# Performance work log

Hardware: AMD Instinct MI355X
Metric: run time of the kernel (lower is better)

Reference implementation:

```python
import jax, jax.numpy as jnp
import numpy as np
from functools import partial

EPS = 1e-3  # keras LayerNormalization default epsilon

def _conv_same(inp, w):
    # inp: [B,H,W,Cin], w: [k,k,Cin,Cout]
    return jax.lax.conv_general_dilated(
        inp, w, window_strides=(1, 1), padding='SAME',
        dimension_numbers=('NHWC', 'HWIO', 'NHWC'))

def _hard_sigmoid(x):
    # keras recurrent_activation default for ConvLSTM2D
    return jnp.clip(0.2 * x + 0.5, 0.0, 1.0)

def setup_inputs() -> dict:
    key = jax.random.key(0)
    k1, k2, k3 = jax.random.split(key, 3)
    B, T, H, W, C, F, K = 4, 16, 64, 64, 32, 64, 3
    x = jax.random.normal(k1, (B, T, H, W, C), dtype=jnp.float32)
    gamma = jnp.ones((C,), jnp.float32)
    beta = jnp.zeros((C,), jnp.float32)
    # gate order i, f, c, o stacked along output channels (keras convention)
    Wx = jax.random.normal(k2, (K, K, C, 4 * F), dtype=jnp.float32) * 0.05
    Wh = jax.random.normal(k3, (K, K, F, 4 * F), dtype=jnp.float32) * 0.05
    b = jnp.zeros((4 * F,), jnp.float32)
    return {"x": x, "gamma": gamma, "beta": beta, "Wx": Wx, "Wh": Wh, "b": b}

def reference(x, gamma, beta, Wx, Wh, b):
    B, T, H, W, C = x.shape
    F = Wh.shape[2]
    # LayerNorm over channel axis
    mu = jnp.mean(x, axis=-1, keepdims=True)
    var = jnp.var(x, axis=-1, keepdims=True)
    xn = (x - mu) * jax.lax.rsqrt(var + EPS) * gamma + beta

    # Precompute input-to-gate convs for all timesteps at once (time folded into batch)
    zx = _conv_same(xn.reshape(B * T, H, W, C), Wx) + b  # [B*T,H,W,4F]
    zx = zx.reshape(B, T, H, W, 4 * F).transpose(1, 0, 2, 3, 4)  # [T,B,H,W,4F]

    def step(carry, zxt):
        h, c = carry
        z = zxt + _conv_same(h, Wh)
        zi, zf, zc, zo = jnp.split(z, 4, axis=-1)
        i = _hard_sigmoid(zi)
        f = _hard_sigmoid(zf)
        c = f * c + i * jnp.tanh(zc)
        o = _hard_sigmoid(zo)
        h = o * jnp.tanh(c)
        return (h, c), h

    h0 = jnp.zeros((B, H, W, F), x.dtype)
    c0 = jnp.zeros((B, H, W, F), x.dtype)
    _, hs = jax.lax.scan(step, (h0, c0), zx)  # hs: [T,B,H,W,F]
    y = hs.transpose(1, 0, 2, 3, 4)  # [B,T,H,W,F] (return_sequences=True)

    # MaxPool3D pool_size=(1,2,2), stride = pool_size, VALID padding
    y = jax.lax.reduce_window(
        y, -jnp.inf, jax.lax.max,
        window_dimensions=(1, 1, 2, 2, 1),
        window_strides=(1, 1, 2, 2, 1),
        padding='VALID')
    return y
```

## Files before the change

### kernel.cpp

```cpp
#include <hip/hip_runtime.h>
#include <hip/hip_fp16.h>

typedef _Float16 f16;
typedef _Float16 f16x8 __attribute__((ext_vector_type(8)));
typedef float f32x4 __attribute__((ext_vector_type(4)));
typedef unsigned long long ull;

#define BB 4
#define TT 16
#define HH 64
#define WW 64
#define CC 32
#define FF 64
#define GG 256

__device__ __forceinline__ float hsig(float z) {
    return fminf(fmaxf(0.2f * z + 0.5f, 0.f), 1.f);
}
__device__ __forceinline__ float tanh_fast(float x) {
    return 1.f - 2.f / (__expf(2.f * x) + 1.f);
}

__device__ __forceinline__ void async_copy16(const void* g, void* l) {
    __builtin_amdgcn_global_load_lds(
        (const __attribute__((address_space(1))) unsigned*)g,
        (__attribute__((address_space(3))) unsigned*)l, 16, 0, 0);
}

__global__ void wprep_kernel(const float* __restrict__ wx, const float* __restrict__ wh,
                             f16* __restrict__ wcat) {
    int e = blockIdx.x * 256 + threadIdx.x;
    if (e < 9 * CC * GG) {
        int n = e & 255, k = e >> 8;
        int p = k / 96, r = k % 96;
        wcat[((p * 12 + (r >> 3)) * 256 + n) * 8 + (r & 7)] = (f16)wx[e];
    } else {
        e -= 9 * CC * GG;
        if (e < 9 * FF * GG) {
            int n = e & 255, k = 288 + (e >> 8);
            int p = k / 96, r = k % 96;
            wcat[((p * 12 + (r >> 3)) * 256 + n) * 8 + (r & 7)] = (f16)wh[e];
        }
    }
}

__global__ __launch_bounds__(512, 2)
void fused_kernel(const float* __restrict__ x, const float* __restrict__ gamma,
                  const float* __restrict__ beta, const f16* __restrict__ wcat,
                  const float* __restrict__ bs, f16* __restrict__ halo,
                  float* __restrict__ out, unsigned* __restrict__ flags) {
    __shared__ __align__(16) f16 patches[3 * 7200];
    __shared__ __align__(16) f16 wbuf[2 * 24576];
    __shared__ float sg[CC], sb[CC];

    f16* xpatch = patches;
    int tid = threadIdx.x;
    int tile = blockIdx.x;
    int bb = tile >> 6, ty = (tile >> 3) & 7, tx = tile & 7;
    int lane = tid & 63, w = tid >> 6;
    int wm = w >> 2, nhalf = (w >> 1) & 1, wn = w & 1;
    int quad = lane >> 4, noff = lane & 15;

    if (tid < CC) sg[tid] = gamma[tid];
    else if (tid < 2 * CC) sb[tid - CC] = beta[tid - CC];

    for (int i = tid; i < 2700; i += 512)
        ((f16x8*)patches)[i] = (f16x8){0, 0, 0, 0, 0, 0, 0, 0};

    const char* gw[6];
#pragma unroll
    for (int i = 0; i < 6; i++) {
        int g = w * 6 + i;
        gw[i] = (const char*)wcat + ((size_t)(g >> 2) * 256 + (g & 3) * 64 + lane) * 16;
    }

    int fch = (nhalf << 5) + (wn << 4) + noff;
    float b_i = bs[fch], b_f = bs[64 + fch], b_c = bs[128 + fch], b_o = bs[192 + fch];

    float creg[2][4];
#pragma unroll
    for (int mt = 0; mt < 2; mt++)
#pragma unroll
        for (int r = 0; r < 4; r++) creg[mt][r] = 0.f;

    int mrow[2];
#pragma unroll
    for (int mt = 0; mt < 2; mt++) {
        int m = (wm << 5) + (mt << 4) + noff;
        mrow[mt] = ((m >> 3) * 10 + (m & 7)) * 72 + (quad << 3);
    }
    int rB[4];
#pragma unroll
    for (int cls = 0; cls < 4; cls++) rB[cls] = ((cls << 6) + fch) << 3;

    __syncthreads();

#pragma unroll
    for (int i = 0; i < 6; i++) {
        int g = w * 6 + i;
        async_copy16(gw[i], &wbuf[(g >> 2) * 2048 + (g & 3) * 512]);
    }

    for (int t = 0; t < TT; t++) {
        f16* hp_cur = patches + 7200 + (t & 1) * 7200;
        f16* hp_nxt = patches + 7200 + ((t + 1) & 1) * 7200;
        f16* wrd0 = &wbuf[(t & 1) * 24576];
        f16* wrd1 = &wbuf[((t + 1) & 1) * 24576];

        if (tid < 200) {
            int pix = tid >> 1, part = tid & 1;
            int py = pix / 10, px_ = pix % 10;
            int gy = ty * 8 - 1 + py, gx = tx * 8 - 1 + px_;
            if (gy >= 0 && gy < HH && gx >= 0 && gx < WW) {
                const float* xp = x + ((size_t)(bb * TT + t) * (HH * WW)
                                       + gy * WW + gx) * CC + part * 16;
                float v[16];
                float s = 0.f, s2 = 0.f;
#pragma unroll
                for (int j = 0; j < 4; j++) {
                    float4 t4 = *(const float4*)(xp + j * 4);
                    v[j * 4] = t4.x; v[j * 4 + 1] = t4.y; v[j * 4 + 2] = t4.z; v[j * 4 + 3] = t4.w;
                    s += t4.x + t4.y + t4.z + t4.w;
                    s2 += t4.x * t4.x + t4.y * t4.y + t4.z * t4.z + t4.w * t4.w;
                }
                s += __shfl_xor(s, 1);
                s2 += __shfl_xor(s2, 1);
                float mu = s * (1.f / CC);
                float var = s2 * (1.f / CC) - mu * mu;
                float rs = rsqrtf(var + 1e-3f);
                f16 o16[16];
#pragma unroll
                for (int c = 0; c < 16; c++)
                    o16[c] = (f16)((v[c] - mu) * rs * sg[part * 16 + c] + sb[part * 16 + c]);
                f16x8* d = (f16x8*)&xpatch[pix * 72 + part * 16];
                d[0] = *(f16x8*)&o16[0];
                d[1] = *(f16x8*)&o16[8];
            }
        }

        f32x4 acc[2][4];
#pragma unroll
        for (int i = 0; i < 2; i++)
#pragma unroll
            for (int j = 0; j < 4; j++) acc[i][j] = (f32x4){0.f, 0.f, 0.f, 0.f};

#pragma unroll
        for (int p = 0; p < 9; ++p) {
            __syncthreads();
            {
                int nc = (p == 8) ? 0 : p + 1;
                f16* wdst = (p & 1) ? wrd0 : wrd1;
#pragma unroll
                for (int i = 0; i < 6; i++) {
                    int g = w * 6 + i;
                    async_copy16(gw[i] + (size_t)nc * 49152,
                                 &wdst[(g >> 2) * 2048 + (g & 3) * 512]);
                }
            }
            const f16* wbp = (p & 1) ? wrd1 : wrd0;
#pragma unroll
            for (int cw = 0; cw < 3; ++cw) {
                int c = p * 3 + cw;
                bool isx = c < 9;
                int hc = c - 9;
                int tap = isx ? c : (hc >> 1);
                int coff = isx ? 0 : ((hc & 1) << 5);
                const f16* ap = isx ? xpatch : hp_cur;
                int dy = tap / 3, dx = tap % 3;
                int toff = (dy * 10 + dx) * 72 + coff;
                f16x8 a[2];
#pragma unroll
                for (int mt = 0; mt < 2; mt++)
                    a[mt] = *(const f16x8*)&ap[mrow[mt] + toff];
#pragma unroll
                for (int cls = 0; cls < 4; cls++) {
                    f16x8 bf = *(const f16x8*)&wbp[((cw << 2) + quad) * 2048 + rB[cls]];
                    acc[0][cls] = __builtin_amdgcn_mfma_f32_16x16x32_f16(a[0], bf, acc[0][cls], 0, 0, 0);
                    acc[1][cls] = __builtin_amdgcn_mfma_f32_16x16x32_f16(a[1], bf, acc[1][cls], 0, 0, 0);
                }
            }
            if (p == 2 && t > 0 && tid >= 256 && tid < 400) {
                int e = tid - 256;
                int hx = e >> 2, quarter = e & 3;
                int py, px_;
                if (hx < 10)      { py = 0; px_ = hx; }
                else if (hx < 20) { py = 9; px_ = hx - 10; }
                else if (hx < 28) { py = 1 + (hx - 20); px_ = 0; }
                else              { py = 1 + (hx - 28); px_ = 9; }
                int gy = ty * 8 - 1 + py, gx = tx * 8 - 1 + px_;
                if (gy >= 0 && gy < HH && gx >= 0 && gx < WW) {
                    int nb = bb * 64 + ((gy >> 3) << 3) + (gx >> 3);
                    while (__hip_atomic_load(&flags[nb], __ATOMIC_RELAXED,
                                             __HIP_MEMORY_SCOPE_AGENT) < (unsigned)t)
                        __builtin_amdgcn_s_sleep(1);
                    const ull* src = (const ull*)(halo + ((size_t)(t * BB + bb) * (HH * WW)
                                                         + gy * WW + gx) * FF) + quarter * 4;
                    f16* dst = &hp_cur[(py * 10 + px_) * 72 + quarter * 16];
#pragma unroll
                    for (int j = 0; j < 4; j++) {
                        ull vv = __hip_atomic_load(src + j, __ATOMIC_RELAXED,
                                                   __HIP_MEMORY_SCOPE_AGENT);
                        *(ull*)(dst + j * 4) = vv;
                    }
                }
            }
        }

#pragma unroll
        for (int mt = 0; mt < 2; mt++) {
#pragma unroll
            for (int r = 0; r < 4; r++) {
                int m = (wm << 5) + (mt << 4) + (quad << 2) + r;
                int py8 = m >> 3, px8 = m & 7;
                float zi = acc[mt][0][r] + b_i;
                float zf = acc[mt][1][r] + b_f;
                float zc = acc[mt][2][r] + b_c;
                float zo = acc[mt][3][r] + b_o;
                float ig = hsig(zi), fg = hsig(zf), og = hsig(zo);
                float cn = fg * creg[mt][r] + ig * tanh_fast(zc);
                creg[mt][r] = cn;
                f16 hval = (f16)(og * tanh_fast(cn));
                hp_nxt[((py8 + 1) * 10 + px8 + 1) * 72 + fch] = hval;
                if (py8 == 0 || py8 == 7 || px8 == 0 || px8 == 7) {
                    union { f16 f; unsigned short u; } cvt; cvt.f = hval;
                    unsigned short* hp = (unsigned short*)halo
                        + ((size_t)((t + 1) * BB + bb) * (HH * WW)
                           + (ty * 8 + py8) * WW + (tx * 8 + px8)) * FF + fch;
                    __hip_atomic_store(hp, cvt.u, __ATOMIC_RELAXED, __HIP_MEMORY_SCOPE_AGENT);
                }
            }
        }
        __syncthreads();
        if (tid == 0)
            __hip_atomic_store(&flags[tile], (unsigned)(t + 1), __ATOMIC_RELAXED,
                               __HIP_MEMORY_SCOPE_AGENT);

        {
            int o = tid * 2;
            int f0 = o & 63;
            int ox2 = (o >> 6) & 3, oy2 = (o >> 8) & 3;
            int row = 1 + oy2 * 2, col = 1 + ox2 * 2;
            const f16* hb = &hp_nxt[(row * 10 + col) * 72 + f0];
            float v0 = fmaxf(fmaxf((float)hb[0], (float)hb[72]),
                             fmaxf((float)hb[720], (float)hb[792]));
            float v1 = fmaxf(fmaxf((float)hb[1], (float)hb[73]),
                             fmaxf((float)hb[721], (float)hb[793]));
            size_t ofs = (((size_t)(bb * TT + t) * 32 + (ty * 4 + oy2)) * 32
                          + (tx * 4 + ox2)) * 64 + f0;
            float2 v2; v2.x = v0; v2.y = v1;
            *(float2*)(out + ofs) = v2;
        }
    }
}

__global__ void ln_kernel(const float* __restrict__ x,
                          const float* __restrict__ gamma,
                          const float* __restrict__ beta,
                          f16* __restrict__ xn) {
    __shared__ float sg[CC], sb[CC];
    if (threadIdx.x < CC) sg[threadIdx.x] = gamma[threadIdx.x];
    else if (threadIdx.x < 2 * CC) sb[threadIdx.x - CC] = beta[threadIdx.x - CC];
    __syncthreads();
    int q = blockIdx.x * 256 + threadIdx.x;
    const float* xp = x + (size_t)q * CC;
    float v[CC];
    float s = 0.f, s2 = 0.f;
#pragma unroll
    for (int c = 0; c < CC; c += 4) {
        float4 t4 = *(const float4*)(xp + c);
        v[c] = t4.x; v[c + 1] = t4.y; v[c + 2] = t4.z; v[c + 3] = t4.w;
        s += t4.x + t4.y + t4.z + t4.w;
        s2 += t4.x * t4.x + t4.y * t4.y + t4.z * t4.z + t4.w * t4.w;
    }
    float mu = s * (1.f / CC);
    float var = s2 * (1.f / CC) - mu * mu;
    float rs = rsqrtf(var + 1e-3f);
    f16 o[CC];
#pragma unroll
    for (int c = 0; c < CC; c++)
        o[c] = (f16)((v[c] - mu) * rs * sg[c] + sb[c]);
    f16x8* d = (f16x8*)(xn + (size_t)q * CC);
#pragma unroll
    for (int c = 0; c < 4; c++) d[c] = *(f16x8*)&o[c * 8];
}

__global__ __launch_bounds__(256, 2)
void step_kernel(const f16* __restrict__ xn, const f16* __restrict__ wcat,
                 const float* __restrict__ bs,
                 float* __restrict__ cst, f16* __restrict__ hs, int t) {
    __shared__ __align__(16) f16 xpatch[100 * 72];
    __shared__ __align__(16) f16 hpatch[100 * 72];
    __shared__ __align__(16) f16 wbuf[2 * 12288];

    int tile = blockIdx.x >> 1, nhalf = blockIdx.x & 1;
    int bb = tile >> 6, ty = (tile >> 3) & 7, tx = tile & 7;
    int tid = threadIdx.x;
    int lane = tid & 63, w = tid >> 6;
    int wm = w >> 1, wn = w & 1;
    int quad = lane >> 4, noff = lane & 15;

    const char* gw[6];
#pragma unroll
    for (int i = 0; i < 6; i++) {
        int g = w * 6 + i;
        int hb = g & 1;
        int gate = (((hb << 1) + (lane >> 5)) << 6) + (nhalf << 5) + (lane & 31);
        gw[i] = (const char*)wcat + ((size_t)(g >> 1) * 256 + gate) * 16;
    }
#pragma unroll
    for (int i = 0; i < 6; i++) {
        int g = w * 6 + i;
        async_copy16(gw[i], &wbuf[(g >> 1) * 1024 + (g & 1) * 512]);
    }

    const f16* xslice = xn + (size_t)(bb * TT + t) * (HH * WW) * CC;
    const f16* hprev = hs + (size_t)t * (BB * HH * WW * FF);
    f16* hnew = hs + (size_t)(t + 1) * (BB * HH * WW * FF);

    if (tid < 200) {
        int pix = tid >> 1, part = tid & 1;
        int py = pix / 10, px = pix % 10;
        int y = ty * 8 - 1 + py, x = tx * 8 - 1 + px;
        bool in = (y >= 0 && y < HH && x >= 0 && x < WW);
        f16x8 z = {0, 0, 0, 0, 0, 0, 0, 0};
        {
            f16x8* d = (f16x8*)&xpatch[pix * 72 + part * 16];
            if (in) {
                const f16x8* s = (const f16x8*)(xslice + ((size_t)y * WW + x) * CC + part * 16);
                d[0] = s[0]; d[1] = s[1];
            } else { d[0] = z; d[1] = z; }
        }
        {
            f16x8* d = (f16x8*)&hpatch[pix * 72 + part * 32];
            if (in) {
                const f16x8* s = (const f16x8*)(hprev + ((size_t)(bb * HH + y) * WW + x) * FF + part * 32);
                d[0] = s[0]; d[1] = s[1]; d[2] = s[2]; d[3] = s[3];
            } else { d[0] = z; d[1] = z; d[2] = z; d[3] = z; }
        }
    }

    int fch = (nhalf << 5) + (wn << 4) + noff;
    float b_i = bs[fch], b_f = bs[64 + fch], b_c = bs[128 + fch], b_o = bs[192 + fch];

    f32x4 acc[2][4];
#pragma unroll
    for (int i = 0; i < 2; i++)
#pragma unroll
        for (int j = 0; j < 4; j++) acc[i][j] = (f32x4){0.f, 0.f, 0.f, 0.f};

#pragma unroll
    for (int p = 0; p < 9; ++p) {
        __syncthreads();
        if (p < 8) {
#pragma unroll
            for (int i = 0; i < 6; i++) {
                int g = w * 6 + i;
                async_copy16(gw[i] + (size_t)(p + 1) * 49152,
                             &wbuf[((p + 1) & 1) * 12288 + (g >> 1) * 1024 + (g & 1) * 512]);
            }
        }
        const f16* wb = &wbuf[(p & 1) * 12288];
#pragma unroll
        for (int cw = 0; cw < 3; ++cw) {
            int c = p * 3 + cw;
            bool isx = c < 9;
            int hc = c - 9;
            int tap = isx ? c : (hc >> 1);
            int coff = isx ? 0 : ((hc & 1) << 5);
            const f16* ap = isx ? xpatch : hpatch;
            int dy = tap / 3, dx = tap % 3;
            f16x8 a[2];
#pragma unroll
            for (int mt = 0; mt < 2; mt++) {
                int m = (wm << 5) + (mt << 4) + noff;
                int pp = ((m >> 3) + dy) * 10 + (m & 7) + dx;
                a[mt] = *(const f16x8*)&ap[pp * 72 + coff + (quad << 3)];
            }
#pragma unroll
            for (int cls = 0; cls < 4; cls++) {
                f16x8 bf = *(const f16x8*)&wb[((cw << 2) + quad) * 1024 + (((cls << 5) + (wn << 4) + noff) << 3)];
                acc[0][cls] = __builtin_amdgcn_mfma_f32_16x16x32_f16(a[0], bf, acc[0][cls], 0, 0, 0);
                acc[1][cls] = __builtin_amdgcn_mfma_f32_16x16x32_f16(a[1], bf, acc[1][cls], 0, 0, 0);
            }
        }
    }

#pragma unroll
    for (int mt = 0; mt < 2; mt++) {
#pragma unroll
        for (int r = 0; r < 4; r++) {
            int m = (wm << 5) + (mt << 4) + (quad << 2) + r;
            int y = ty * 8 + (m >> 3), x = tx * 8 + (m & 7);
            size_t p = (size_t)(bb * HH + y) * WW + x;
            float zi = acc[mt][0][r] + b_i;
            float zf = acc[mt][1][r] + b_f;
            float zc = acc[mt][2][r] + b_c;
            float zo = acc[mt][3][r] + b_o;
            float ig = hsig(zi), fg = hsig(zf), og = hsig(zo);
            float cold = cst[p * FF + fch];
            float cn = fg * cold + ig * tanh_fast(zc);
            cst[p * FF + fch] = cn;
            hnew[p * FF + fch] = (f16)(og * tanh_fast(cn));
        }
    }
}

__global__ void pool_kernel(const f16* __restrict__ hs, float* __restrict__ out) {
    int idx = blockIdx.x * 256 + threadIdx.x;
    int f = idx & 63;
    int ox = (idx >> 6) & 31;
    int oy = (idx >> 11) & 31;
    int t = (idx >> 16) & 15;
    int bb = idx >> 20;
    const f16* base = hs + (size_t)(t + 1) * (BB * HH * WW * FF)
                    + ((size_t)(bb * HH + oy * 2) * WW + ox * 2) * FF + f;
    float v0 = (float)base[0];
    float v1 = (float)base[FF];
    float v2 = (float)base[WW * FF];
    float v3 = (float)base[WW * FF + FF];
    out[idx] = fmaxf(fmaxf(v0, v1), fmaxf(v2, v3));
}

extern "C" void kernel_launch(void* const* d_in, const int* in_sizes, int n_in,
                              void* d_out, int out_size, void* d_ws, size_t ws_size,
                              hipStream_t stream) {
    const float* x = (const float*)d_in[0];
    const float* gamma = (const float*)d_in[1];
    const float* beta = (const float*)d_in[2];
    const float* wx = (const float*)d_in[3];
    const float* wh = (const float*)d_in[4];
    const float* bs = (const float*)d_in[5];
    float* out = (float*)d_out;

    char* ws = (char*)d_ws;
    f16* xn = (f16*)ws;
    f16* wcat = (f16*)(ws + 16777216);
    float* cst = (float*)(ws + 17219584);
    f16* hs = (f16*)(ws + 21413888);
    unsigned* flags = (unsigned*)cst;

    hipMemsetAsync(flags, 0, 256 * 4, stream);
    wprep_kernel<<<864, 256, 0, stream>>>(wx, wh, wcat);

    void* args[8];
    args[0] = (void*)&x;
    args[1] = (void*)&gamma;
    args[2] = (void*)&beta;
    args[3] = (void*)&wcat;
    args[4] = (void*)&bs;
    args[5] = (void*)&hs;
    args[6] = (void*)&out;
    args[7] = (void*)&flags;
    hipError_t err = hipLaunchCooperativeKernel((const void*)fused_kernel, dim3(256),
                                                dim3(512), args, 0, stream);
    if (err != hipSuccess) {
        (void)hipGetLastError();
        hipMemsetAsync(cst, 0, (size_t)BB * HH * WW * FF * 4, stream);
        hipMemsetAsync(hs, 0, (size_t)BB * HH * WW * FF * 2, stream);
        ln_kernel<<<1024, 256, 0, stream>>>(x, gamma, beta, xn);
        for (int t = 0; t < TT; t++)
            step_kernel<<<512, 256, 0, stream>>>(xn, wcat, bs, cst, hs, t);
        pool_kernel<<<16384, 256, 0, stream>>>(hs, out);
    }
}
```

Measured before the change: 295.3 us.

## Split work by gate-channel quarter on 16x16 spatial tiles in fused ConvLSTM

Blocks now own a 16x16 spatial tile and one quarter of the F channels (all four gates for 16 channels), in place of an 8x8 tile covering every channel. The weight layout is split per quarter with an XOR swizzle to avoid LDS bank conflicts. Each block writes its full h to global and reloads the whole 18x18 patch every step, and the max-pool and the next step's LayerNorm staging move into the tap loop. This cuts per-block weight traffic and halo overhead, at the cost of more global h traffic, finer-grained flag waits, and a 4x redundant LayerNorm across the quarter blocks.

```diff
diff --git a/kernel.cpp b/kernel.cpp
--- a/kernel.cpp
+++ b/kernel.cpp
@@ -28,53 +28,86 @@
 }
 
 __global__ void wprep_kernel(const float* __restrict__ wx, const float* __restrict__ wh,
-                             f16* __restrict__ wcat) {
-    int e = blockIdx.x * 256 + threadIdx.x;
-    if (e < 9 * CC * GG) {
-        int n = e & 255, k = e >> 8;
-        int p = k / 96, r = k % 96;
-        wcat[((p * 12 + (r >> 3)) * 256 + n) * 8 + (r & 7)] = (f16)wx[e];
+                             f16* __restrict__ wcatA, f16* __restrict__ wcatB) {
+    int e0 = blockIdx.x * 256 + threadIdx.x;
+    float val; int k, ng;
+    if (e0 < 9 * CC * GG) {
+        ng = e0 & 255; k = e0 >> 8; val = wx[e0];
     } else {
-        e -= 9 * CC * GG;
-        if (e < 9 * FF * GG) {
-            int n = e & 255, k = 288 + (e >> 8);
-            int p = k / 96, r = k % 96;
-            wcat[((p * 12 + (r >> 3)) * 256 + n) * 8 + (r & 7)] = (f16)wh[e];
+        int e = e0 - 9 * CC * GG;
+        ng = e & 255; k = 288 + (e >> 8); val = wh[e];
+    }
+    int p = k / 96, r = k % 96, j = r >> 3, el = r & 7;
+    wcatB[((p * 12 + j) * 256 + ng) * 8 + el] = (f16)val;
+    int q = (ng >> 4) & 3;
+    int n = ((ng >> 6) << 4) | (ng & 15);
+    int slot = n ^ ((j & 3) << 1);
+    wcatA[(((q * 9 + p) * 12 + j) * 64 + slot) * 8 + el] = (f16)val;
+}
+
+__device__ __forceinline__ void stage_x_ln(const float* __restrict__ x, int bb, int t,
+                                           int tY, int tX, int tid,
+                                           const float* sg, const float* sb,
+                                           f16* xpatch) {
+    if (tid < 324) {
+        int py = tid / 18, pxx = tid - py * 18;
+        int gy = tY * 16 - 1 + py, gx = tX * 16 - 1 + pxx;
+        if (gy >= 0 && gy < HH && gx >= 0 && gx < WW) {
+            const float* xp = x + ((size_t)(bb * TT + t) * (HH * WW) + gy * WW + gx) * CC;
+            float v[CC];
+            float s = 0.f, s2 = 0.f;
+#pragma unroll
+            for (int c = 0; c < CC; c += 4) {
+                float4 t4 = *(const float4*)(xp + c);
+                v[c] = t4.x; v[c + 1] = t4.y; v[c + 2] = t4.z; v[c + 3] = t4.w;
+                s += t4.x + t4.y + t4.z + t4.w;
+                s2 += t4.x * t4.x + t4.y * t4.y + t4.z * t4.z + t4.w * t4.w;
+            }
+            float mu = s * (1.f / CC);
+            float var = s2 * (1.f / CC) - mu * mu;
+            float rs = rsqrtf(var + 1e-3f);
+            f16 o[CC];
+#pragma unroll
+            for (int c = 0; c < CC; c++)
+                o[c] = (f16)((v[c] - mu) * rs * sg[c] + sb[c]);
+            *(f16x8*)&xpatch[tid * 40]      = *(f16x8*)&o[0];
+            *(f16x8*)&xpatch[tid * 40 + 8]  = *(f16x8*)&o[8];
+            *(f16x8*)&xpatch[tid * 40 + 16] = *(f16x8*)&o[16];
+            *(f16x8*)&xpatch[tid * 40 + 24] = *(f16x8*)&o[24];
         }
     }
 }
 
 __global__ __launch_bounds__(512, 2)
 void fused_kernel(const float* __restrict__ x, const float* __restrict__ gamma,
-                  const float* __restrict__ beta, const f16* __restrict__ wcat,
+                  const float* __restrict__ beta, const f16* __restrict__ wcatA,
                   const float* __restrict__ bs, f16* __restrict__ halo,
                   float* __restrict__ out, unsigned* __restrict__ flags) {
-    __shared__ __align__(16) f16 patches[3 * 7200];
-    __shared__ __align__(16) f16 wbuf[2 * 24576];
+    __shared__ __align__(16) f16 xpatch[324 * 40];
+    __shared__ __align__(16) f16 hpatch[324 * 72];
+    __shared__ __align__(16) f16 wbuf[2 * 6144];
     __shared__ float sg[CC], sb[CC];
 
-    f16* xpatch = patches;
     int tid = threadIdx.x;
-    int tile = blockIdx.x;
-    int bb = tile >> 6, ty = (tile >> 3) & 7, tx = tile & 7;
+    int bid = blockIdx.x;
+    int Q = bid & 3, tl = bid >> 2;
+    int bb = tl >> 4, tY = (tl >> 2) & 3, tX = tl & 3;
     int lane = tid & 63, w = tid >> 6;
-    int wm = w >> 2, nhalf = (w >> 1) & 1, wn = w & 1;
     int quad = lane >> 4, noff = lane & 15;
 
     if (tid < CC) sg[tid] = gamma[tid];
     else if (tid < 2 * CC) sb[tid - CC] = beta[tid - CC];
 
-    for (int i = tid; i < 2700; i += 512)
-        ((f16x8*)patches)[i] = (f16x8){0, 0, 0, 0, 0, 0, 0, 0};
-
-    const char* gw[6];
-#pragma unroll
-    for (int i = 0; i < 6; i++) {
-        int g = w * 6 + i;
-        gw[i] = (const char*)wcat + ((size_t)(g >> 2) * 256 + (g & 3) * 64 + lane) * 16;
-    }
-
-    int fch = (nhalf << 5) + (wn << 4) + noff;
+    {
+        f16x8 z8 = {0, 0, 0, 0, 0, 0, 0, 0};
+        for (int i = tid; i < 1620; i += 512) ((f16x8*)xpatch)[i] = z8;
+        for (int i = tid; i < 2916; i += 512) ((f16x8*)hpatch)[i] = z8;
+    }
+
+    const char* gw0 = (const char*)wcatA + (size_t)Q * 110592 + w * 1024 + lane * 16;
+    const char* gw1 = gw0 + 8192;
+
+    int fch = (Q << 4) + noff;
     float b_i = bs[fch], b_f = bs[64 + fch], b_c = bs[128 + fch], b_o = bs[192 + fch];
 
     float creg[2][4];
@@ -83,60 +116,23 @@
 #pragma unroll
         for (int r = 0; r < 4; r++) creg[mt][r] = 0.f;
 
-    int mrow[2];
+    int arow[2], hrow[2];
 #pragma unroll
     for (int mt = 0; mt < 2; mt++) {
-        int m = (wm << 5) + (mt << 4) + noff;
-        mrow[mt] = ((m >> 3) * 10 + (m & 7)) * 72 + (quad << 3);
-    }
-    int rB[4];
-#pragma unroll
-    for (int cls = 0; cls < 4; cls++) rB[cls] = ((cls << 6) + fch) << 3;
+        arow[mt] = ((w * 2 + mt) * 18 + noff) * 40 + (quad << 3);
+        hrow[mt] = ((w * 2 + mt) * 18 + noff) * 72 + (quad << 3);
+    }
+    int qB = quad * 512 + ((noff ^ (quad << 1)) << 3);
 
     __syncthreads();
 
-#pragma unroll
-    for (int i = 0; i < 6; i++) {
-        int g = w * 6 + i;
-        async_copy16(gw[i], &wbuf[(g >> 2) * 2048 + (g & 3) * 512]);
-    }
+    async_copy16(gw0, &wbuf[w * 512]);
+    if (w < 4) async_copy16(gw1, &wbuf[4096 + w * 512]);
+    stage_x_ln(x, bb, 0, tY, tX, tid, sg, sb, xpatch);
 
     for (int t = 0; t < TT; t++) {
-        f16* hp_cur = patches + 7200 + (t & 1) * 7200;
-        f16* hp_nxt = patches + 7200 + ((t + 1) & 1) * 7200;
-        f16* wrd0 = &wbuf[(t & 1) * 24576];
-        f16* wrd1 = &wbuf[((t + 1) & 1) * 24576];
-
-        if (tid < 200) {
-            int pix = tid >> 1, part = tid & 1;
-            int py = pix / 10, px_ = pix % 10;
-            int gy = ty * 8 - 1 + py, gx = tx * 8 - 1 + px_;
-            if (gy >= 0 && gy < HH && gx >= 0 && gx < WW) {
-                const float* xp = x + ((size_t)(bb * TT + t) * (HH * WW)
-                                       + gy * WW + gx) * CC + part * 16;
-                float v[16];
-                float s = 0.f, s2 = 0.f;
-#pragma unroll
-                for (int j = 0; j < 4; j++) {
-                    float4 t4 = *(const float4*)(xp + j * 4);
-                    v[j * 4] = t4.x; v[j * 4 + 1] = t4.y; v[j * 4 + 2] = t4.z; v[j * 4 + 3] = t4.w;
-                    s += t4.x + t4.y + t4.z + t4.w;
-                    s2 += t4.x * t4.x + t4.y * t4.y + t4.z * t4.z + t4.w * t4.w;
-                }
-                s += __shfl_xor(s, 1);
-                s2 += __shfl_xor(s2, 1);
-                float mu = s * (1.f / CC);
-                float var = s2 * (1.f / CC) - mu * mu;
-                float rs = rsqrtf(var + 1e-3f);
-                f16 o16[16];
-#pragma unroll
-                for (int c = 0; c < 16; c++)
-                    o16[c] = (f16)((v[c] - mu) * rs * sg[part * 16 + c] + sb[part * 16 + c]);
-                f16x8* d = (f16x8*)&xpatch[pix * 72 + part * 16];
-                d[0] = *(f16x8*)&o16[0];
-                d[1] = *(f16x8*)&o16[8];
-            }
-        }
+        f16* wrd0 = &wbuf[(t & 1) * 6144];
+        f16* wrd1 = &wbuf[((t + 1) & 1) * 6144];
 
         f32x4 acc[2][4];
 #pragma unroll
@@ -150,12 +146,8 @@
             {
                 int nc = (p == 8) ? 0 : p + 1;
                 f16* wdst = (p & 1) ? wrd0 : wrd1;
-#pragma unroll
-                for (int i = 0; i < 6; i++) {
-                    int g = w * 6 + i;
-                    async_copy16(gw[i] + (size_t)nc * 49152,
-                                 &wdst[(g >> 2) * 2048 + (g & 3) * 512]);
-                }
+                async_copy16(gw0 + nc * 12288, &wdst[w * 512]);
+                if (w < 4) async_copy16(gw1 + nc * 12288, &wdst[4096 + w * 512]);
             }
             const f16* wbp = (p & 1) ? wrd1 : wrd0;
 #pragma unroll
@@ -165,53 +157,76 @@
                 int hc = c - 9;
                 int tap = isx ? c : (hc >> 1);
                 int coff = isx ? 0 : ((hc & 1) << 5);
-                const f16* ap = isx ? xpatch : hp_cur;
                 int dy = tap / 3, dx = tap % 3;
-                int toff = (dy * 10 + dx) * 72 + coff;
                 f16x8 a[2];
 #pragma unroll
                 for (int mt = 0; mt < 2; mt++)
-                    a[mt] = *(const f16x8*)&ap[mrow[mt] + toff];
+                    a[mt] = isx
+                        ? *(const f16x8*)&xpatch[arow[mt] + (dy * 18 + dx) * 40]
+                        : *(const f16x8*)&hpatch[hrow[mt] + (dy * 18 + dx) * 72 + coff];
 #pragma unroll
                 for (int cls = 0; cls < 4; cls++) {
-                    f16x8 bf = *(const f16x8*)&wbp[((cw << 2) + quad) * 2048 + rB[cls]];
+                    f16x8 bf = *(const f16x8*)&wbp[qB + cw * 2048 + cls * 128];
                     acc[0][cls] = __builtin_amdgcn_mfma_f32_16x16x32_f16(a[0], bf, acc[0][cls], 0, 0, 0);
                     acc[1][cls] = __builtin_amdgcn_mfma_f32_16x16x32_f16(a[1], bf, acc[1][cls], 0, 0, 0);
                 }
             }
-            if (p == 2 && t > 0 && tid >= 256 && tid < 400) {
-                int e = tid - 256;
-                int hx = e >> 2, quarter = e & 3;
-                int py, px_;
-                if (hx < 10)      { py = 0; px_ = hx; }
-                else if (hx < 20) { py = 9; px_ = hx - 10; }
-                else if (hx < 28) { py = 1 + (hx - 20); px_ = 0; }
-                else              { py = 1 + (hx - 28); px_ = 9; }
-                int gy = ty * 8 - 1 + py, gx = tx * 8 - 1 + px_;
-                if (gy >= 0 && gy < HH && gx >= 0 && gx < WW) {
-                    int nb = bb * 64 + ((gy >> 3) << 3) + (gx >> 3);
-                    while (__hip_atomic_load(&flags[nb], __ATOMIC_RELAXED,
-                                             __HIP_MEMORY_SCOPE_AGENT) < (unsigned)t)
-                        __builtin_amdgcn_s_sleep(1);
-                    const ull* src = (const ull*)(halo + ((size_t)(t * BB + bb) * (HH * WW)
-                                                         + gy * WW + gx) * FF) + quarter * 4;
-                    f16* dst = &hp_cur[(py * 10 + px_) * 72 + quarter * 16];
-#pragma unroll
-                    for (int j = 0; j < 4; j++) {
-                        ull vv = __hip_atomic_load(src + j, __ATOMIC_RELAXED,
-                                                   __HIP_MEMORY_SCOPE_AGENT);
-                        *(ull*)(dst + j * 4) = vv;
+            if (p == 2 && t > 0) {
+#pragma unroll
+                for (int k2 = 0; k2 < 3; k2++) {
+                    int tau = tid + k2 * 512;
+                    if (tau < 1296) {
+                        int pxi = tau >> 2, grp = tau & 3;
+                        int py = pxi / 18, pxx = pxi - py * 18;
+                        int gy = tY * 16 - 1 + py, gx = tX * 16 - 1 + pxx;
+                        if (gy >= 0 && gy < HH && gx >= 0 && gx < WW) {
+                            int nb = ((bb * 16 + (gy >> 4) * 4 + (gx >> 4)) << 2) | grp;
+                            while (__hip_atomic_load(&flags[nb], __ATOMIC_RELAXED,
+                                                     __HIP_MEMORY_SCOPE_AGENT) < (unsigned)t)
+                                __builtin_amdgcn_s_sleep(1);
+                            const ull* src = (const ull*)(halo
+                                + ((size_t)(t * BB + bb) * (HH * WW) + gy * WW + gx) * FF
+                                + grp * 16);
+                            ull v0 = __hip_atomic_load(src, __ATOMIC_RELAXED,
+                                                       __HIP_MEMORY_SCOPE_AGENT);
+                            ull v1 = __hip_atomic_load(src + 1, __ATOMIC_RELAXED,
+                                                       __HIP_MEMORY_SCOPE_AGENT);
+                            ull v2 = __hip_atomic_load(src + 2, __ATOMIC_RELAXED,
+                                                       __HIP_MEMORY_SCOPE_AGENT);
+                            ull v3 = __hip_atomic_load(src + 3, __ATOMIC_RELAXED,
+                                                       __HIP_MEMORY_SCOPE_AGENT);
+                            ull* dst = (ull*)&hpatch[pxi * 72 + grp * 16];
+                            dst[0] = v0; dst[1] = v1; dst[2] = v2; dst[3] = v3;
+                        }
                     }
                 }
             }
+            if (p == 3 && t > 0) {
+                int a_ = tid >> 6, b_ = (tid >> 3) & 7, ch = (tid & 7) << 3;
+                const f16* h00 = &hpatch[((1 + 2 * a_) * 18 + 1 + 2 * b_) * 72 + ch];
+                f16x8 q00 = *(const f16x8*)h00;
+                f16x8 q01 = *(const f16x8*)(h00 + 72);
+                f16x8 q10 = *(const f16x8*)(h00 + 18 * 72);
+                f16x8 q11 = *(const f16x8*)(h00 + 18 * 72 + 72);
+                float o8[8];
+#pragma unroll
+                for (int j = 0; j < 8; j++)
+                    o8[j] = fmaxf(fmaxf((float)q00[j], (float)q01[j]),
+                                  fmaxf((float)q10[j], (float)q11[j]));
+                size_t ofs = ((((size_t)bb * TT + (t - 1)) * 32 + tY * 8 + a_) * 32
+                              + (tX * 8 + b_)) * 64 + ch;
+                *(float4*)(out + ofs) = *(float4*)&o8[0];
+                *(float4*)(out + ofs + 4) = *(float4*)&o8[4];
+            }
+            if (p == 4 && t + 1 < TT)
+                stage_x_ln(x, bb, t + 1, tY, tX, tid, sg, sb, xpatch);
         }
 
 #pragma unroll
         for (int mt = 0; mt < 2; mt++) {
 #pragma unroll
             for (int r = 0; r < 4; r++) {
-                int m = (wm << 5) + (mt << 4) + (quad << 2) + r;
-                int py8 = m >> 3, px8 = m & 7;
+                int gy = tY * 16 + w * 2 + mt, gx = tX * 16 + (quad << 2) + r;
                 float zi = acc[mt][0][r] + b_i;
                 float zf = acc[mt][1][r] + b_f;
                 float zc = acc[mt][2][r] + b_c;
@@ -219,37 +234,47 @@
                 float ig = hsig(zi), fg = hsig(zf), og = hsig(zo);
                 float cn = fg * creg[mt][r] + ig * tanh_fast(zc);
                 creg[mt][r] = cn;
-                f16 hval = (f16)(og * tanh_fast(cn));
-                hp_nxt[((py8 + 1) * 10 + px8 + 1) * 72 + fch] = hval;
-                if (py8 == 0 || py8 == 7 || px8 == 0 || px8 == 7) {
-                    union { f16 f; unsigned short u; } cvt; cvt.f = hval;
-                    unsigned short* hp = (unsigned short*)halo
-                        + ((size_t)((t + 1) * BB + bb) * (HH * WW)
-                           + (ty * 8 + py8) * WW + (tx * 8 + px8)) * FF + fch;
-                    __hip_atomic_store(hp, cvt.u, __ATOMIC_RELAXED, __HIP_MEMORY_SCOPE_AGENT);
-                }
+                union { f16 f; unsigned short u; } cvt;
+                cvt.f = (f16)(og * tanh_fast(cn));
+                unsigned short* hp = (unsigned short*)halo
+                    + ((size_t)((t + 1) * BB + bb) * (HH * WW) + gy * WW + gx) * FF + fch;
+                __hip_atomic_store(hp, cvt.u, __ATOMIC_RELAXED, __HIP_MEMORY_SCOPE_AGENT);
             }
         }
         __syncthreads();
         if (tid == 0)
-            __hip_atomic_store(&flags[tile], (unsigned)(t + 1), __ATOMIC_RELAXED,
+            __hip_atomic_store(&flags[bid], (unsigned)(t + 1), __ATOMIC_RELAXED,
                                __HIP_MEMORY_SCOPE_AGENT);
-
-        {
-            int o = tid * 2;
-            int f0 = o & 63;
-            int ox2 = (o >> 6) & 3, oy2 = (o >> 8) & 3;
-            int row = 1 + oy2 * 2, col = 1 + ox2 * 2;
-            const f16* hb = &hp_nxt[(row * 10 + col) * 72 + f0];
-            float v0 = fmaxf(fmaxf((float)hb[0], (float)hb[72]),
-                             fmaxf((float)hb[720], (float)hb[792]));
-            float v1 = fmaxf(fmaxf((float)hb[1], (float)hb[73]),
-                             fmaxf((float)hb[721], (float)hb[793]));
-            size_t ofs = (((size_t)(bb * TT + t) * 32 + (ty * 4 + oy2)) * 32
-                          + (tx * 4 + ox2)) * 64 + f0;
-            float2 v2; v2.x = v0; v2.y = v1;
-            *(float2*)(out + ofs) = v2;
-        }
+    }
+
+    if (tid < 4) {
+        while (__hip_atomic_load(&flags[(tl << 2) | tid], __ATOMIC_RELAXED,
+                                 __HIP_MEMORY_SCOPE_AGENT) < (unsigned)TT)
+            __builtin_amdgcn_s_sleep(2);
+    }
+    __syncthreads();
+    {
+        int a_ = tid >> 6, b_ = (tid >> 3) & 7, ch = (tid & 7) << 3;
+        float o8[8];
+#pragma unroll
+        for (int j = 0; j < 8; j++) o8[j] = -1e30f;
+#pragma unroll
+        for (int dy2 = 0; dy2 < 2; dy2++)
+#pragma unroll
+            for (int dx2 = 0; dx2 < 2; dx2++) {
+                int gy = tY * 16 + 2 * a_ + dy2, gx = tX * 16 + 2 * b_ + dx2;
+                const ull* src = (const ull*)(halo
+                    + ((size_t)(TT * BB + bb) * (HH * WW) + gy * WW + gx) * FF + ch);
+                ull v0 = __hip_atomic_load(src, __ATOMIC_RELAXED, __HIP_MEMORY_SCOPE_AGENT);
+                ull v1 = __hip_atomic_load(src + 1, __ATOMIC_RELAXED, __HIP_MEMORY_SCOPE_AGENT);
+                f16 tmp[8];
+                *(ull*)&tmp[0] = v0; *(ull*)&tmp[4] = v1;
+#pragma unroll
+                for (int j = 0; j < 8; j++) o8[j] = fmaxf(o8[j], (float)tmp[j]);
+            }
+        size_t ofs = ((((size_t)bb * TT + 15) * 32 + tY * 8 + a_) * 32 + (tX * 8 + b_)) * 64 + ch;
+        *(float4*)(out + ofs) = *(float4*)&o8[0];
+        *(float4*)(out + ofs + 4) = *(float4*)&o8[4];
     }
 }
 
@@ -434,19 +459,20 @@
 
     char* ws = (char*)d_ws;
     f16* xn = (f16*)ws;
-    f16* wcat = (f16*)(ws + 16777216);
+    f16* wcatB = (f16*)(ws + 16777216);
     float* cst = (float*)(ws + 17219584);
     f16* hs = (f16*)(ws + 21413888);
+    f16* wcatA = (f16*)(ws + 57065472);
     unsigned* flags = (unsigned*)cst;
 
     hipMemsetAsync(flags, 0, 256 * 4, stream);
-    wprep_kernel<<<864, 256, 0, stream>>>(wx, wh, wcat);
+    wprep_kernel<<<864, 256, 0, stream>>>(wx, wh, wcatA, wcatB);
 
     void* args[8];
     args[0] = (void*)&x;
     args[1] = (void*)&gamma;
     args[2] = (void*)&beta;
-    args[3] = (void*)&wcat;
+    args[3] = (void*)&wcatA;
     args[4] = (void*)&bs;
     args[5] = (void*)&hs;
     args[6] = (void*)&out;
@@ -459,7 +485,7 @@
         hipMemsetAsync(hs, 0, (size_t)BB * HH * WW * FF * 2, stream);
         ln_kernel<<<1024, 256, 0, stream>>>(x, gamma, beta, xn);
         for (int t = 0; t < TT; t++)
-            step_kernel<<<512, 256, 0, stream>>>(xn, wcat, bs, cst, hs, t);
+            step_kernel<<<512, 256, 0, stream>>>(xn, wcatB, bs, cst, hs, t);
         pool_kernel<<<16384, 256, 0, stream>>>(hs, out);
     }
 }
```

Result: slower. 332.2 us (+12.5%).

## Swizzle weight layout in LDS and prefetch next-step LayerNorm x-patch mid-step

Applied to the files above, without the earlier changes.

Adds a second, XOR-swizzled weight copy (wcatF) whose slot index is permuted by the K-chunk, so that B-fragment reads from LDS by different quads hit different banks. The fused kernel reads B through the matching swizzled offsets, while the fallback path keeps the original layout. LayerNorm staging of the next timestep's x patch moves from the start of each step to the middle of the tap loop (after p==4, once the x taps are consumed), to overlap global loads with MFMA work. This needs another workspace region and relies on the x patch no longer being read after p==2.

```diff
diff --git a/kernel.cpp b/kernel.cpp
--- a/kernel.cpp
+++ b/kernel.cpp
@@ -28,25 +28,60 @@
 }
 
 __global__ void wprep_kernel(const float* __restrict__ wx, const float* __restrict__ wh,
-                             f16* __restrict__ wcat) {
-    int e = blockIdx.x * 256 + threadIdx.x;
-    if (e < 9 * CC * GG) {
-        int n = e & 255, k = e >> 8;
-        int p = k / 96, r = k % 96;
-        wcat[((p * 12 + (r >> 3)) * 256 + n) * 8 + (r & 7)] = (f16)wx[e];
+                             f16* __restrict__ wcatF, f16* __restrict__ wcatB) {
+    int e0 = blockIdx.x * 256 + threadIdx.x;
+    float val; int k, ng;
+    if (e0 < 9 * CC * GG) {
+        ng = e0 & 255; k = e0 >> 8; val = wx[e0];
     } else {
-        e -= 9 * CC * GG;
-        if (e < 9 * FF * GG) {
-            int n = e & 255, k = 288 + (e >> 8);
-            int p = k / 96, r = k % 96;
-            wcat[((p * 12 + (r >> 3)) * 256 + n) * 8 + (r & 7)] = (f16)wh[e];
+        int e = e0 - 9 * CC * GG;
+        ng = e & 255; k = 288 + (e >> 8); val = wh[e];
+    }
+    int p = k / 96, r = k % 96, j = r >> 3, el = r & 7;
+    wcatB[((p * 12 + j) * 256 + ng) * 8 + el] = (f16)val;
+    int slot = ng ^ ((j & 3) << 1);
+    wcatF[((p * 12 + j) * 256 + slot) * 8 + el] = (f16)val;
+}
+
+__device__ __forceinline__ void stage_x_ln(const float* __restrict__ x, int bb, int t,
+                                           int ty, int tx, int tid,
+                                           const float* sg, const float* sb,
+                                           f16* __restrict__ xpatch) {
+    if (tid < 200) {
+        int pix = tid >> 1, part = tid & 1;
+        int py = pix / 10, px_ = pix % 10;
+        int gy = ty * 8 - 1 + py, gx = tx * 8 - 1 + px_;
+        if (gy >= 0 && gy < HH && gx >= 0 && gx < WW) {
+            const float* xp = x + ((size_t)(bb * TT + t) * (HH * WW)
+                                   + gy * WW + gx) * CC + part * 16;
+            float v[16];
+            float s = 0.f, s2 = 0.f;
+#pragma unroll
+            for (int j = 0; j < 4; j++) {
+                float4 t4 = *(const float4*)(xp + j * 4);
+                v[j * 4] = t4.x; v[j * 4 + 1] = t4.y; v[j * 4 + 2] = t4.z; v[j * 4 + 3] = t4.w;
+                s += t4.x + t4.y + t4.z + t4.w;
+                s2 += t4.x * t4.x + t4.y * t4.y + t4.z * t4.z + t4.w * t4.w;
+            }
+            s += __shfl_xor(s, 1);
+            s2 += __shfl_xor(s2, 1);
+            float mu = s * (1.f / CC);
+            float var = s2 * (1.f / CC) - mu * mu;
+            float rs = rsqrtf(var + 1e-3f);
+            f16 o16[16];
+#pragma unroll
+            for (int c = 0; c < 16; c++)
+                o16[c] = (f16)((v[c] - mu) * rs * sg[part * 16 + c] + sb[part * 16 + c]);
+            f16x8* d = (f16x8*)&xpatch[pix * 72 + part * 16];
+            d[0] = *(f16x8*)&o16[0];
+            d[1] = *(f16x8*)&o16[8];
         }
     }
 }
 
 __global__ __launch_bounds__(512, 2)
 void fused_kernel(const float* __restrict__ x, const float* __restrict__ gamma,
-                  const float* __restrict__ beta, const f16* __restrict__ wcat,
+                  const float* __restrict__ beta, const f16* __restrict__ wcatF,
                   const float* __restrict__ bs, f16* __restrict__ halo,
                   float* __restrict__ out, unsigned* __restrict__ flags) {
     __shared__ __align__(16) f16 patches[3 * 7200];
@@ -71,7 +106,7 @@
 #pragma unroll
     for (int i = 0; i < 6; i++) {
         int g = w * 6 + i;
-        gw[i] = (const char*)wcat + ((size_t)(g >> 2) * 256 + (g & 3) * 64 + lane) * 16;
+        gw[i] = (const char*)wcatF + ((size_t)(g >> 2) * 256 + (g & 3) * 64 + lane) * 16;
     }
 
     int fch = (nhalf << 5) + (wn << 4) + noff;
@@ -89,9 +124,10 @@
         int m = (wm << 5) + (mt << 4) + noff;
         mrow[mt] = ((m >> 3) * 10 + (m & 7)) * 72 + (quad << 3);
     }
-    int rB[4];
-#pragma unroll
-    for (int cls = 0; cls < 4; cls++) rB[cls] = ((cls << 6) + fch) << 3;
+    int rBx[4];
+#pragma unroll
+    for (int cls = 0; cls < 4; cls++)
+        rBx[cls] = ((((cls << 6) + fch) ^ (quad << 1)) << 3);
 
     __syncthreads();
 
@@ -100,43 +136,13 @@
         int g = w * 6 + i;
         async_copy16(gw[i], &wbuf[(g >> 2) * 2048 + (g & 3) * 512]);
     }
+    stage_x_ln(x, bb, 0, ty, tx, tid, sg, sb, xpatch);
 
     for (int t = 0; t < TT; t++) {
         f16* hp_cur = patches + 7200 + (t & 1) * 7200;
         f16* hp_nxt = patches + 7200 + ((t + 1) & 1) * 7200;
         f16* wrd0 = &wbuf[(t & 1) * 24576];
         f16* wrd1 = &wbuf[((t + 1) & 1) * 24576];
-
-        if (tid < 200) {
-            int pix = tid >> 1, part = tid & 1;
-            int py = pix / 10, px_ = pix % 10;
-            int gy = ty * 8 - 1 + py, gx = tx * 8 - 1 + px_;
-            if (gy >= 0 && gy < HH && gx >= 0 && gx < WW) {
-                const float* xp = x + ((size_t)(bb * TT + t) * (HH * WW)
-                                       + gy * WW + gx) * CC + part * 16;
-                float v[16];
-                float s = 0.f, s2 = 0.f;
-#pragma unroll
-                for (int j = 0; j < 4; j++) {
-                    float4 t4 = *(const float4*)(xp + j * 4);
-                    v[j * 4] = t4.x; v[j * 4 + 1] = t4.y; v[j * 4 + 2] = t4.z; v[j * 4 + 3] = t4.w;
-                    s += t4.x + t4.y + t4.z + t4.w;
-                    s2 += t4.x * t4.x + t4.y * t4.y + t4.z * t4.z + t4.w * t4.w;
-                }
-                s += __shfl_xor(s, 1);
-                s2 += __shfl_xor(s2, 1);
-                float mu = s * (1.f / CC);
-                float var = s2 * (1.f / CC) - mu * mu;
-                float rs = rsqrtf(var + 1e-3f);
-                f16 o16[16];
-#pragma unroll
-                for (int c = 0; c < 16; c++)
-                    o16[c] = (f16)((v[c] - mu) * rs * sg[part * 16 + c] + sb[part * 16 + c]);
-                f16x8* d = (f16x8*)&xpatch[pix * 72 + part * 16];
-                d[0] = *(f16x8*)&o16[0];
-                d[1] = *(f16x8*)&o16[8];
-            }
-        }
 
         f32x4 acc[2][4];
 #pragma unroll
@@ -174,7 +180,7 @@
                     a[mt] = *(const f16x8*)&ap[mrow[mt] + toff];
 #pragma unroll
                 for (int cls = 0; cls < 4; cls++) {
-                    f16x8 bf = *(const f16x8*)&wbp[((cw << 2) + quad) * 2048 + rB[cls]];
+                    f16x8 bf = *(const f16x8*)&wbp[((cw << 2) + quad) * 2048 + rBx[cls]];
                     acc[0][cls] = __builtin_amdgcn_mfma_f32_16x16x32_f16(a[0], bf, acc[0][cls], 0, 0, 0);
                     acc[1][cls] = __builtin_amdgcn_mfma_f32_16x16x32_f16(a[1], bf, acc[1][cls], 0, 0, 0);
                 }
@@ -204,6 +210,8 @@
                     }
                 }
             }
+            if (p == 4 && t + 1 < TT)
+                stage_x_ln(x, bb, t + 1, ty, tx, tid, sg, sb, xpatch);
         }
 
 #pragma unroll
@@ -434,19 +442,20 @@
 
     char* ws = (char*)d_ws;
     f16* xn = (f16*)ws;
-    f16* wcat = (f16*)(ws + 16777216);
+    f16* wcatB = (f16*)(ws + 16777216);
     float* cst = (float*)(ws + 17219584);
     f16* hs = (f16*)(ws + 21413888);
+    f16* wcatF = (f16*)(ws + 57065472);
     unsigned* flags = (unsigned*)cst;
 
     hipMemsetAsync(flags, 0, 256 * 4, stream);
-    wprep_kernel<<<864, 256, 0, stream>>>(wx, wh, wcat);
+    wprep_kernel<<<864, 256, 0, stream>>>(wx, wh, wcatF, wcatB);
 
     void* args[8];
     args[0] = (void*)&x;
     args[1] = (void*)&gamma;
     args[2] = (void*)&beta;
-    args[3] = (void*)&wcat;
+    args[3] = (void*)&wcatF;
     args[4] = (void*)&bs;
     args[5] = (void*)&hs;
     args[6] = (void*)&out;
@@ -459,7 +468,7 @@
         hipMemsetAsync(hs, 0, (size_t)BB * HH * WW * FF * 2, stream);
         ln_kernel<<<1024, 256, 0, stream>>>(x, gamma, beta, xn);
         for (int t = 0; t < TT; t++)
-            step_kernel<<<512, 256, 0, stream>>>(xn, wcat, bs, cst, hs, t);
+            step_kernel<<<512, 256, 0, stream>>>(xn, wcatB, bs, cst, hs, t);
         pool_kernel<<<16384, 256, 0, stream>>>(hs, out);
     }
 }
```

New measurement: 351.9 us. 1.19x slower.
